# Performance work log

Hardware: AMD Instinct MI355X
Metric: run time of the kernel (lower is better)

## Reference

```python
import jax, jax.numpy as jnp
import numpy as np

B, N, FEAT = 64, 1024, 3
HID, STATE, LAYERS, NTYPES = 64, 32, 2, 10


def setup_inputs() -> dict:
    key = jax.random.key(0)
    ks = jax.random.split(key, 16)
    s = 0.1
    return {
        "task_features": jax.random.normal(ks[0], (B, N, FEAT), jnp.float32),
        "task_types": jax.random.randint(ks[1], (B, N), 0, NTYPES, jnp.int32),
        "prev_state": jnp.zeros((B, STATE), jnp.float32),
        "enc_w1": jax.random.normal(ks[2], (HID, FEAT), jnp.float32) * s,
        "enc_b1": jnp.zeros((HID,), jnp.float32),
        "enc_w2": jax.random.normal(ks[3], (HID, HID), jnp.float32) * s,
        "enc_b2": jnp.zeros((HID,), jnp.float32),
        "contention": jax.random.normal(ks[4], (NTYPES, NTYPES), jnp.float32) * 0.1,
        "gnn_w": jax.random.normal(ks[5], (LAYERS, HID, HID), jnp.float32) * s,
        "gnn_b": jnp.zeros((LAYERS, HID), jnp.float32),
        "gru_w_ih": jax.random.normal(ks[6], (3 * STATE, HID), jnp.float32) * s,
        "gru_w_hh": jax.random.normal(ks[7], (3 * STATE, STATE), jnp.float32) * s,
        "gru_b_ih": jnp.zeros((3 * STATE,), jnp.float32),
        "gru_b_hh": jnp.zeros((3 * STATE,), jnp.float32),
        "head_w1": jax.random.normal(ks[8], (HID, HID + STATE), jnp.float32) * s,
        "head_b1": jnp.zeros((HID,), jnp.float32),
        "head_w2": jax.random.normal(ks[9], (1, HID), jnp.float32) * s,
        "head_b2": jnp.zeros((1,), jnp.float32),
    }


def _forward(task_features, task_types, prev_state, enc_w1, enc_b1, enc_w2, enc_b2,
             contention, gnn_w, gnn_b, gru_w_ih, gru_w_hh, gru_b_ih, gru_b_hh,
             head_w1, head_b1, head_w2, head_b2):
    # task encoder: Linear -> ReLU -> Linear
    emb = jax.nn.relu(task_features @ enc_w1.T + enc_b1) @ enc_w2.T + enc_b2  # (B,N,H)
    # interaction graph: type-pair gather + cosine similarity
    base = contention[task_types[:, :, None], task_types[:, None, :]]  # (B,N,N)
    nrm = emb / jnp.maximum(jnp.linalg.norm(emb, axis=-1, keepdims=True), 1e-12)
    sim = jnp.einsum("bnd,bmd->bnm", nrm, nrm)
    adjacency = jax.nn.sigmoid(base) * sim  # (B,N,N)
    # GNN layers: aggregate + linear + relu
    h = emb
    for l in range(LAYERS):
        agg = jnp.einsum("bnm,bmd->bnd", adjacency, h)
        h = jax.nn.relu((h + agg) @ gnn_w[l].T + gnn_b[l])
    ctx = h.mean(axis=1)  # (B,H)
    # GRUCell (torch semantics)
    gi = ctx @ gru_w_ih.T + gru_b_ih
    gh = prev_state @ gru_w_hh.T + gru_b_hh
    i_r, i_z, i_n = jnp.split(gi, 3, axis=-1)
    h_r, h_z, h_n = jnp.split(gh, 3, axis=-1)
    r = jax.nn.sigmoid(i_r + h_r)
    z = jax.nn.sigmoid(i_z + h_z)
    n = jnp.tanh(i_n + r * h_n)
    new_state = (1.0 - z) * n + z * prev_state  # (B,S)
    # latency head on [h, state]
    st = jnp.broadcast_to(new_state[:, None, :], (h.shape[0], h.shape[1], new_state.shape[-1]))
    combined = jnp.concatenate([h, st], axis=-1)
    lat = jax.nn.relu(combined @ head_w1.T + head_b1) @ head_w2.T + head_b2
    return lat[..., 0], new_state


def reference(task_features, task_types, prev_state, enc_w1, enc_b1, enc_w2, enc_b2,
              contention, gnn_w, gnn_b, gru_w_ih, gru_w_hh, gru_b_ih, gru_b_hh,
              head_w1, head_b1, head_w2, head_b2):
    return _forward(task_features, task_types, prev_state, enc_w1, enc_b1, enc_w2, enc_b2,
                    contention, gnn_w, gnn_b, gru_w_ih, gru_w_hh, gru_b_ih, gru_b_hh,
                    head_w1, head_b1, head_w2, head_b2)
```

## Files before the change

### kernel.cpp

```cpp
#include <hip/hip_runtime.h>
#include <math.h>

#define BB 64
#define NN 1024
#define HID 64
#define STATE 32
#define NTYPES 10

typedef _Float16 f16;
typedef f16 f16x8 __attribute__((ext_vector_type(8)));
typedef f16 f16x4 __attribute__((ext_vector_type(4)));
typedef float f32x4 __attribute__((ext_vector_type(4)));

#define MFMA16(a, b, c) __builtin_amdgcn_mfma_f32_16x16x32_f16(a, b, c, 0, 0, 0)

__device__ __forceinline__ float sigm(float x) { return 1.f / (1.f + expf(-x)); }

__device__ __forceinline__ f16x8 cvt8(float4 a, float4 b) {
    f16x8 r;
    r[0] = (f16)a.x; r[1] = (f16)a.y; r[2] = (f16)a.z; r[3] = (f16)a.w;
    r[4] = (f16)b.x; r[5] = (f16)b.y; r[6] = (f16)b.z; r[7] = (f16)b.w;
    return r;
}
__device__ __forceinline__ unsigned packh2(f16 a, f16 b) {
    union { f16 h[2]; unsigned u; } p;
    p.h[0] = a; p.h[1] = b;
    return p.u;
}

__global__ __launch_bounds__(256) void k_misc(
    const float* __restrict__ w2, const float* __restrict__ gw,
    const float* __restrict__ hw1, f16* __restrict__ out,
    int* __restrict__ cnt, float* __restrict__ ctx)
{
    int p = blockIdx.x * 256 + threadIdx.x;
    if (p < 18432) {
        const float* W; int K, pl;
        if (p < 12288) { int seg = p >> 12; pl = p & 4095; W = (seg == 0) ? w2 : gw + (seg - 1) * 4096; K = 64; }
        else { W = hw1; K = 96; pl = p - 12288; }
        int j = pl & 7, lane = (pl >> 3) & 63, nt = (pl >> 9) & 3, ch = pl >> 11;
        int k = ch * 32 + ((lane >> 4) << 3) + j;
        int o = nt * 16 + (lane & 15);
        out[p] = (f16)W[o * K + k];
        return;
    }
    int q = p - 18432;
    if (q < BB * NTYPES) { cnt[q] = 0; return; }
    q -= BB * NTYPES;
    if (q < BB * HID) ctx[q] = 0.f;
}

__global__ __launch_bounds__(256) void k_encoder(
    const float* __restrict__ feat,
    const float* __restrict__ w1, const float* __restrict__ b1,
    const f16* __restrict__ w2f, const float* __restrict__ b2,
    const int* __restrict__ types, int* __restrict__ idx, int* __restrict__ cnt,
    f16* __restrict__ nrm, float* __restrict__ sclv)
{
    __shared__ f16 w2s[4096];
    __shared__ f16 tmp[4][16 * 72];
    __shared__ float fbuf[4][48];
    int tid = threadIdx.x, wave = tid >> 6, lane = tid & 63;
    int l15 = lane & 15, quad = lane >> 4;
    if (tid < 64) {
        int row = blockIdx.x * 64 + tid;
        int b = row >> 10;
        int t = types[row];
        int pos = atomicAdd(&cnt[b * NTYPES + t], 1);
        idx[(b * NTYPES + t) * NN + pos] = row & (NN - 1);
    }
    { const uint4* s = (const uint4*)w2f; uint4* d = (uint4*)w2s;
      for (int i = tid; i < 512; i += 256) d[i] = s[i]; }
    float w10 = w1[lane * 3], w11 = w1[lane * 3 + 1], w12 = w1[lane * 3 + 2], b1l = b1[lane];
    int tb = blockIdx.x * 64 + wave * 16;
    if (lane < 48) fbuf[wave][lane] = feat[tb * 3 + lane];
    __syncthreads();
    f16* tw = &tmp[wave][0];
#pragma unroll
    for (int r = 0; r < 16; ++r) {
        float x0 = fbuf[wave][r * 3], x1 = fbuf[wave][r * 3 + 1], x2 = fbuf[wave][r * 3 + 2];
        float hv = fmaxf(fmaf(w10, x0, fmaf(w11, x1, fmaf(w12, x2, b1l))), 0.f);
        tw[r * 72 + lane] = (f16)hv;
    }
    __builtin_amdgcn_sched_barrier(0);
    f16x8 a0 = *(const f16x8*)&tw[l15 * 72 + quad * 8];
    f16x8 a1 = *(const f16x8*)&tw[l15 * 72 + 32 + quad * 8];
    const f16x8* bf = (const f16x8*)w2s;
    f32x4 acc[4];
#pragma unroll
    for (int nt = 0; nt < 4; ++nt) {
        f32x4 c = {0.f, 0.f, 0.f, 0.f};
        c = MFMA16(a0, bf[(0 * 4 + nt) * 64 + lane], c);
        c = MFMA16(a1, bf[(1 * 4 + nt) * 64 + lane], c);
        acc[nt] = c;
    }
    float b2c[4];
#pragma unroll
    for (int nt = 0; nt < 4; ++nt) b2c[nt] = b2[nt * 16 + l15];
#pragma unroll
    for (int i = 0; i < 4; ++i) {
        float v[4]; float ss = 0.f;
#pragma unroll
        for (int nt = 0; nt < 4; ++nt) { v[nt] = acc[nt][i] + b2c[nt]; ss = fmaf(v[nt], v[nt], ss); }
        ss += __shfl_xor(ss, 1, 64); ss += __shfl_xor(ss, 2, 64);
        ss += __shfl_xor(ss, 4, 64); ss += __shfl_xor(ss, 8, 64);
        float nm = fmaxf(sqrtf(ss), 1e-12f);
        float rinv = 1.f / nm;
        int grow = tb + quad * 4 + i;
#pragma unroll
        for (int nt = 0; nt < 4; ++nt)
            nrm[(size_t)grow * 64 + nt * 16 + l15] = (f16)(v[nt] * rinv);
        if (l15 == 0) sclv[grow] = nm;
    }
}

#define TSTR 40
__global__ __launch_bounds__(256) void k_buildM(
    const int* __restrict__ idx, const int* __restrict__ cnt,
    const f16* __restrict__ nrm, const f16* __restrict__ h,
    const float* __restrict__ scale, f16* __restrict__ M)
{
    __shared__ f16 nT[64 * TSTR];
    __shared__ f16 hT[64 * TSTR];
    int bj = blockIdx.x;
    int b = bj / NTYPES, j = bj % NTYPES;
    int c = cnt[b * NTYPES + j];
    const int* lst = idx + (size_t)bj * NN;
    int tid = threadIdx.x, wave = tid >> 6, lane = tid & 63;
    int l15 = lane & 15, quad = lane >> 4;
    int r = tid & 15;
    int q4 = tid >> 4;
    const f16* nb = nrm + (size_t)b * NN * 64;
    const f16* hb = h + (size_t)b * NN * 64;
    const float* sb = scale ? scale + (size_t)b * NN : nullptr;
    f32x4 acc[4] = {{0.f,0.f,0.f,0.f},{0.f,0.f,0.f,0.f},{0.f,0.f,0.f,0.f},{0.f,0.f,0.f,0.f}};
    for (int k0 = 0; k0 < c; k0 += 32) {
        __syncthreads();
        int m0i = k0 + 2 * r, m1i = m0i + 1;
        f16x4 a0 = {0,0,0,0}, a1 = {0,0,0,0}, g0 = {0,0,0,0}, g1 = {0,0,0,0};
        if (m0i < c) {
            int m = lst[m0i];
            a0 = *(const f16x4*)&nb[(size_t)m * 64 + 4 * q4];
            if (sb) { f16 sm = (f16)sb[m]; f16x4 sv = {sm, sm, sm, sm}; g0 = a0 * sv; }
            else g0 = *(const f16x4*)&hb[(size_t)m * 64 + 4 * q4];
        }
        if (m1i < c) {
            int m = lst[m1i];
            a1 = *(const f16x4*)&nb[(size_t)m * 64 + 4 * q4];
            if (sb) { f16 sm = (f16)sb[m]; f16x4 sv = {sm, sm, sm, sm}; g1 = a1 * sv; }
            else g1 = *(const f16x4*)&hb[(size_t)m * 64 + 4 * q4];
        }
#pragma unroll
        for (int i = 0; i < 4; ++i) {
            *(unsigned*)&nT[(4 * q4 + i) * TSTR + 2 * r] = packh2(a0[i], a1[i]);
            *(unsigned*)&hT[(4 * q4 + i) * TSTR + 2 * r] = packh2(g0[i], g1[i]);
        }
        __syncthreads();
        f16x8 af = *(const f16x8*)&nT[(wave * 16 + l15) * TSTR + quad * 8];
#pragma unroll
        for (int nt = 0; nt < 4; ++nt) {
            f16x8 bfv = *(const f16x8*)&hT[(nt * 16 + l15) * TSTR + quad * 8];
            acc[nt] = MFMA16(af, bfv, acc[nt]);
        }
    }
    f16* Mo = M + (size_t)bj * 4096;
#pragma unroll
    for (int nt = 0; nt < 4; ++nt)
#pragma unroll
        for (int i = 0; i < 4; ++i)
            Mo[(wave * 16 + quad * 4 + i) * 64 + nt * 16 + l15] = (f16)acc[nt][i];
}

__global__ __launch_bounds__(256) void k_gnn_layer(
    const int* __restrict__ idx, const int* __restrict__ cnt,
    const float* __restrict__ cont, const f16* __restrict__ M,
    const f16* __restrict__ nrm, const f16* __restrict__ h,
    const float* __restrict__ scale,
    const f16* __restrict__ gwf, const float* __restrict__ gb,
    f16* __restrict__ hout, float* __restrict__ ctx)
{
    __shared__ f16 ds_[4096];
    __shared__ f16 gs[4096];
    int bt = blockIdx.x;
    int b = bt / NTYPES, t = bt % NTYPES;
    int c = cnt[bt];
    if (c == 0) return;
    int tid = threadIdx.x, wave = tid >> 6, lane = tid & 63;
    int l15 = lane & 15, quad = lane >> 4;
    { const uint4* s2 = (const uint4*)gwf; uint4* d2 = (uint4*)gs;
      for (int i = tid; i < 512; i += 256) d2[i] = s2[i]; }
    float sg[NTYPES];
#pragma unroll
    for (int j = 0; j < NTYPES; ++j) sg[j] = sigm(cont[t * NTYPES + j]);
    float ca[16];
#pragma unroll
    for (int i = 0; i < 16; ++i) ca[i] = 0.f;
    const f16* Mb = M + (size_t)b * NTYPES * 4096;
#pragma unroll
    for (int j = 0; j < NTYPES; ++j) {
        const f16* Mr = Mb + j * 4096 + (wave * 16 + l15) * 64;
        f16x8 m0 = *(const f16x8*)&Mr[quad * 8];
        f16x8 m1 = *(const f16x8*)&Mr[32 + quad * 8];
        float s = sg[j];
#pragma unroll
        for (int e = 0; e < 8; ++e) {
            ca[e]     = fmaf(s, (float)m0[e], ca[e]);
            ca[8 + e] = fmaf(s, (float)m1[e], ca[8 + e]);
        }
    }
    f16x8 ca0, ca1;
#pragma unroll
    for (int i = 0; i < 8; ++i) { ca0[i] = (f16)ca[i]; ca1[i] = (f16)ca[8 + i]; }
    __syncthreads();
    const f16x8* gbf = (const f16x8*)gs;
#pragma unroll
    for (int nt = 0; nt < 4; ++nt) {
        f32x4 dd = {0.f, 0.f, 0.f, 0.f};
        dd = MFMA16(ca0, gbf[(0 * 4 + nt) * 64 + lane], dd);
        dd = MFMA16(ca1, gbf[(1 * 4 + nt) * 64 + lane], dd);
#pragma unroll
        for (int i = 0; i < 4; ++i) {
            int d = wave * 16 + quad * 4 + i;
            int pos = (((d >> 5) * 4 + nt) * 64 + ((d >> 3) & 3) * 16 + l15) * 8 + (d & 7);
            ds_[pos] = (f16)dd[i];
        }
    }
    __syncthreads();
    float gbl[4];
#pragma unroll
    for (int nt = 0; nt < 4; ++nt) gbl[nt] = gb[nt * 16 + l15];
    const int* lst = idx + (size_t)bt * NN;
    const f16* nb = nrm + (size_t)b * NN * 64;
    const f16* hb = h + (size_t)b * NN * 64;
    const float* sb = scale ? scale + (size_t)b * NN : nullptr;
    f16* hob = hout + (size_t)b * NN * 64;
    const f16x8* dbf = (const f16x8*)ds_;
    float cacc[4] = {0.f, 0.f, 0.f, 0.f};
    for (int g = wave; g * 16 < c; g += 4) {
        int tb = g * 16;
        int rA = tb + l15; if (rA >= c) rA = c - 1;
        int mA = lst[rA];
        const f16* na = nb + (size_t)mA * 64;
        f16x8 a0 = *(const f16x8*)&na[quad * 8];
        f16x8 a1 = *(const f16x8*)&na[32 + quad * 8];
        if (sb) {
            f32x4 acc1[4], acc2[4];
#pragma unroll
            for (int nt = 0; nt < 4; ++nt) {
                f32x4 c1 = {0.f, 0.f, 0.f, 0.f}, c2 = {0.f, 0.f, 0.f, 0.f};
                c1 = MFMA16(a0, dbf[(0 * 4 + nt) * 64 + lane], c1);
                c1 = MFMA16(a1, dbf[(1 * 4 + nt) * 64 + lane], c1);
                c2 = MFMA16(a0, gbf[(0 * 4 + nt) * 64 + lane], c2);
                c2 = MFMA16(a1, gbf[(1 * 4 + nt) * 64 + lane], c2);
                acc1[nt] = c1; acc2[nt] = c2;
            }
#pragma unroll
            for (int i = 0; i < 4; ++i) {
                int rr = tb + quad * 4 + i;
                if (rr < c) {
                    int m = lst[rr];
                    float sm = sb[m];
#pragma unroll
                    for (int nt = 0; nt < 4; ++nt) {
                        float v = fmaxf(fmaf(sm, acc2[nt][i], acc1[nt][i]) + gbl[nt], 0.f);
                        hob[(size_t)m * 64 + nt * 16 + l15] = (f16)v;
                        cacc[nt] += v;
                    }
                }
            }
        } else {
            const f16* ha = hb + (size_t)mA * 64;
            f16x8 h0 = *(const f16x8*)&ha[quad * 8];
            f16x8 h1 = *(const f16x8*)&ha[32 + quad * 8];
            f32x4 acc[4];
#pragma unroll
            for (int nt = 0; nt < 4; ++nt) {
                f32x4 cc = {0.f, 0.f, 0.f, 0.f};
                cc = MFMA16(a0, dbf[(0 * 4 + nt) * 64 + lane], cc);
                cc = MFMA16(a1, dbf[(1 * 4 + nt) * 64 + lane], cc);
                cc = MFMA16(h0, gbf[(0 * 4 + nt) * 64 + lane], cc);
                cc = MFMA16(h1, gbf[(1 * 4 + nt) * 64 + lane], cc);
                acc[nt] = cc;
            }
#pragma unroll
            for (int i = 0; i < 4; ++i) {
                int rr = tb + quad * 4 + i;
                if (rr < c) {
                    int m = lst[rr];
#pragma unroll
                    for (int nt = 0; nt < 4; ++nt) {
                        float v = fmaxf(acc[nt][i] + gbl[nt], 0.f);
                        hob[(size_t)m * 64 + nt * 16 + l15] = (f16)v;
                        cacc[nt] += v;
                    }
                }
            }
        }
    }
    if (ctx) {
#pragma unroll
        for (int nt = 0; nt < 4; ++nt) {
            float sv = cacc[nt];
            sv += __shfl_xor(sv, 16, 64);
            sv += __shfl_xor(sv, 32, 64);
            if (quad == 0) atomicAdd(&ctx[b * HID + nt * 16 + l15], sv);
        }
    }
}

__global__ __launch_bounds__(256) void k_head(
    const f16* __restrict__ h2, const float* __restrict__ ctx_sum,
    const float* __restrict__ prev,
    const float* __restrict__ w_ih, const float* __restrict__ w_hh,
    const float* __restrict__ b_ih, const float* __restrict__ b_hh,
    const f16* __restrict__ hwf, const float* __restrict__ b1,
    const float* __restrict__ w2, const float* __restrict__ b2,
    float* __restrict__ lat, float* __restrict__ state_out)
{
    __shared__ f16 ws_[6144];
    __shared__ __align__(16) float st[STATE];
    __shared__ float cs[HID], ps[STATE], gis[96], ghs[96];
    int tid = threadIdx.x, wave = tid >> 6, lane = tid & 63;
    int l15 = lane & 15, quad = lane >> 4;
    int b = blockIdx.x >> 4;
    { const uint4* s = (const uint4*)hwf; uint4* d = (uint4*)ws_;
      for (int i = tid; i < 768; i += 256) d[i] = s[i]; }
    if (tid < HID) cs[tid] = ctx_sum[b * HID + tid] * (1.f / NN);
    if (tid >= HID && tid < HID + STATE) ps[tid - HID] = prev[b * STATE + tid - HID];
    __syncthreads();
    if (tid < 96) {
        float gi = b_ih[tid];
#pragma unroll 8
        for (int k = 0; k < HID; ++k) gi = fmaf(w_ih[tid * HID + k], cs[k], gi);
        float gh = b_hh[tid];
#pragma unroll
        for (int k = 0; k < STATE; ++k) gh = fmaf(w_hh[tid * STATE + k], ps[k], gh);
        gis[tid] = gi; ghs[tid] = gh;
    }
    __syncthreads();
    if (tid < STATE) {
        float r = sigm(gis[tid] + ghs[tid]);
        float z = sigm(gis[32 + tid] + ghs[32 + tid]);
        float nn = tanhf(gis[64 + tid] + r * ghs[64 + tid]);
        float v = (1.f - z) * nn + z * ps[tid];
        st[tid] = v;
        if ((blockIdx.x & 15) == 0) state_out[b * STATE + tid] = v;
    }
    __syncthreads();
    float b1c[4], w2c[4];
#pragma unroll
    for (int nt = 0; nt < 4; ++nt) { b1c[nt] = b1[nt * 16 + l15]; w2c[nt] = w2[nt * 16 + l15]; }
    float b2v = b2[0];
    int tb = blockIdx.x * 64 + wave * 16;
    int grow = tb + l15;
    const f16* ha = h2 + (size_t)grow * 64;
    f16x8 a0 = *(const f16x8*)&ha[quad * 8];
    f16x8 a1 = *(const f16x8*)&ha[32 + quad * 8];
    const float4* sp = (const float4*)st;
    f16x8 a2 = cvt8(sp[quad * 2], sp[quad * 2 + 1]);
    const f16x8* bf = (const f16x8*)ws_;
    f32x4 acc[4];
#pragma unroll
    for (int nt = 0; nt < 4; ++nt) {
        f32x4 cc = {0.f, 0.f, 0.f, 0.f};
        cc = MFMA16(a0, bf[(0 * 4 + nt) * 64 + lane], cc);
        cc = MFMA16(a1, bf[(1 * 4 + nt) * 64 + lane], cc);
        cc = MFMA16(a2, bf[(2 * 4 + nt) * 64 + lane], cc);
        acc[nt] = cc;
    }
#pragma unroll
    for (int i = 0; i < 4; ++i) {
        float s = 0.f;
#pragma unroll
        for (int nt = 0; nt < 4; ++nt) s = fmaf(fmaxf(acc[nt][i] + b1c[nt], 0.f), w2c[nt], s);
        s += __shfl_xor(s, 1, 64); s += __shfl_xor(s, 2, 64);
        s += __shfl_xor(s, 4, 64); s += __shfl_xor(s, 8, 64);
        if (l15 == 0) lat[tb + quad * 4 + i] = s + b2v;
    }
}

extern "C" void kernel_launch(void* const* d_in, const int* in_sizes, int n_in,
                              void* d_out, int out_size, void* d_ws, size_t ws_size,
                              hipStream_t stream) {
    const float* feat   = (const float*)d_in[0];
    const int*   types  = (const int*)d_in[1];
    const float* prev   = (const float*)d_in[2];
    const float* enc_w1 = (const float*)d_in[3];
    const float* enc_b1 = (const float*)d_in[4];
    const float* enc_w2 = (const float*)d_in[5];
    const float* enc_b2 = (const float*)d_in[6];
    const float* cont   = (const float*)d_in[7];
    const float* gnn_w  = (const float*)d_in[8];
    const float* gnn_b  = (const float*)d_in[9];
    const float* w_ih   = (const float*)d_in[10];
    const float* w_hh   = (const float*)d_in[11];
    const float* b_ih   = (const float*)d_in[12];
    const float* b_hh   = (const float*)d_in[13];
    const float* hw1    = (const float*)d_in[14];
    const float* hb1    = (const float*)d_in[15];
    const float* hw2    = (const float*)d_in[16];
    const float* hb2    = (const float*)d_in[17];
    float* out = (float*)d_out;

    float* ws  = (float*)d_ws;
    f16*   nrm = (f16*)ws;
    f16*   h1  = (f16*)(ws + 2097152);
    f16*   h2  = (f16*)(ws + 4194304);
    float* scl = ws + 6291456;
    int*   idx = (int*)(ws + 6356992);
    int*   cnt = idx + BB * NTYPES * NN;
    f16*   M0  = (f16*)(ws + 7012992);
    f16*   M1  = (f16*)(ws + 8323712);
    f16*   wfrag = (f16*)(ws + 9634432);
    float* ctx   = ws + 9643648;
    f16*   w2f  = wfrag;
    f16*   gw0f = wfrag + 4096;
    f16*   gw1f = wfrag + 8192;
    f16*   hwf  = wfrag + 12288;

    k_misc<<<91, 256, 0, stream>>>(enc_w2, gnn_w, hw1, wfrag, cnt, ctx);
    k_encoder<<<BB * NN / 64, 256, 0, stream>>>(feat, enc_w1, enc_b1, w2f, enc_b2,
                                                types, idx, cnt, nrm, scl);
    k_buildM<<<BB * NTYPES, 256, 0, stream>>>(idx, cnt, nrm, nrm, scl, M0);
    k_gnn_layer<<<BB * NTYPES, 256, 0, stream>>>(idx, cnt, cont, M0, nrm, nrm, scl,
                                                 gw0f, gnn_b, h1, nullptr);
    k_buildM<<<BB * NTYPES, 256, 0, stream>>>(idx, cnt, nrm, h1, nullptr, M1);
    k_gnn_layer<<<BB * NTYPES, 256, 0, stream>>>(idx, cnt, cont, M1, nrm, h1, nullptr,
                                                 gw1f, gnn_b + HID, h2, ctx);
    k_head<<<BB * NN / 64, 256, 0, stream>>>(h2, ctx, prev, w_ih, w_hh, b_ih, b_hh,
                                             hwf, hb1, hw2, hb2, out, out + BB * NN);
}
```

Baseline: 183.2 us.

## Fuse head first-layer projection into last GNN layer, split GNN blocks, widen buildM K-tile

The last GNN layer now multiplies its output rows by the head's first 64 weight columns via an extra MFMA pass, staged through a per-wave LDS tile, and stores that projection instead of h2. The head kernel then only adds a per-batch state projection, applies ReLU and takes a dot product, with no MFMA or weight staging. GNN layer launches double the grid, with two blocks per (batch, type) sharing the row groups, and buildM processes 64 neighbours per iteration. The risks are that each doubled block recomputes the type-aggregate setup and that the extra LDS round trip adds latency in the GNN kernel.

```diff
diff --git a/kernel.cpp b/kernel.cpp
--- a/kernel.cpp
+++ b/kernel.cpp
@@ -16,12 +16,6 @@
 
 __device__ __forceinline__ float sigm(float x) { return 1.f / (1.f + expf(-x)); }
 
-__device__ __forceinline__ f16x8 cvt8(float4 a, float4 b) {
-    f16x8 r;
-    r[0] = (f16)a.x; r[1] = (f16)a.y; r[2] = (f16)a.z; r[3] = (f16)a.w;
-    r[4] = (f16)b.x; r[5] = (f16)b.y; r[6] = (f16)b.z; r[7] = (f16)b.w;
-    return r;
-}
 __device__ __forceinline__ unsigned packh2(f16 a, f16 b) {
     union { f16 h[2]; unsigned u; } p;
     p.h[0] = a; p.h[1] = b;
@@ -114,17 +108,17 @@
     }
 }
 
-#define TSTR 40
+#define TSTR2 72
 __global__ __launch_bounds__(256) void k_buildM(
     const int* __restrict__ idx, const int* __restrict__ cnt,
     const f16* __restrict__ nrm, const f16* __restrict__ h,
     const float* __restrict__ scale, f16* __restrict__ M)
 {
-    __shared__ f16 nT[64 * TSTR];
-    __shared__ f16 hT[64 * TSTR];
+    __shared__ f16 nT[64 * TSTR2];
+    __shared__ f16 hT[64 * TSTR2];
     int bj = blockIdx.x;
-    int b = bj / NTYPES, j = bj % NTYPES;
-    int c = cnt[b * NTYPES + j];
+    int b = bj / NTYPES;
+    int c = cnt[bj];
     const int* lst = idx + (size_t)bj * NN;
     int tid = threadIdx.x, wave = tid >> 6, lane = tid & 63;
     int l15 = lane & 15, quad = lane >> 4;
@@ -134,33 +128,37 @@
     const f16* hb = h + (size_t)b * NN * 64;
     const float* sb = scale ? scale + (size_t)b * NN : nullptr;
     f32x4 acc[4] = {{0.f,0.f,0.f,0.f},{0.f,0.f,0.f,0.f},{0.f,0.f,0.f,0.f},{0.f,0.f,0.f,0.f}};
-    for (int k0 = 0; k0 < c; k0 += 32) {
+    for (int k0 = 0; k0 < c; k0 += 64) {
         __syncthreads();
-        int m0i = k0 + 2 * r, m1i = m0i + 1;
-        f16x4 a0 = {0,0,0,0}, a1 = {0,0,0,0}, g0 = {0,0,0,0}, g1 = {0,0,0,0};
-        if (m0i < c) {
-            int m = lst[m0i];
-            a0 = *(const f16x4*)&nb[(size_t)m * 64 + 4 * q4];
-            if (sb) { f16 sm = (f16)sb[m]; f16x4 sv = {sm, sm, sm, sm}; g0 = a0 * sv; }
-            else g0 = *(const f16x4*)&hb[(size_t)m * 64 + 4 * q4];
-        }
-        if (m1i < c) {
-            int m = lst[m1i];
-            a1 = *(const f16x4*)&nb[(size_t)m * 64 + 4 * q4];
-            if (sb) { f16 sm = (f16)sb[m]; f16x4 sv = {sm, sm, sm, sm}; g1 = a1 * sv; }
-            else g1 = *(const f16x4*)&hb[(size_t)m * 64 + 4 * q4];
+        f16x4 a[4], g[4];
+#pragma unroll
+        for (int u = 0; u < 4; ++u) { a[u] = (f16x4){0,0,0,0}; g[u] = (f16x4){0,0,0,0}; }
+#pragma unroll
+        for (int u = 0; u < 4; ++u) {
+            int mi = k0 + 4 * r + u;
+            if (mi < c) {
+                int m = lst[mi];
+                a[u] = *(const f16x4*)&nb[(size_t)m * 64 + 4 * q4];
+                if (sb) { f16 sm = (f16)sb[m]; f16x4 sv = {sm, sm, sm, sm}; g[u] = a[u] * sv; }
+                else g[u] = *(const f16x4*)&hb[(size_t)m * 64 + 4 * q4];
+            }
         }
 #pragma unroll
         for (int i = 0; i < 4; ++i) {
-            *(unsigned*)&nT[(4 * q4 + i) * TSTR + 2 * r] = packh2(a0[i], a1[i]);
-            *(unsigned*)&hT[(4 * q4 + i) * TSTR + 2 * r] = packh2(g0[i], g1[i]);
+            *(unsigned*)&nT[(4 * q4 + i) * TSTR2 + 4 * r]     = packh2(a[0][i], a[1][i]);
+            *(unsigned*)&nT[(4 * q4 + i) * TSTR2 + 4 * r + 2] = packh2(a[2][i], a[3][i]);
+            *(unsigned*)&hT[(4 * q4 + i) * TSTR2 + 4 * r]     = packh2(g[0][i], g[1][i]);
+            *(unsigned*)&hT[(4 * q4 + i) * TSTR2 + 4 * r + 2] = packh2(g[2][i], g[3][i]);
         }
         __syncthreads();
-        f16x8 af = *(const f16x8*)&nT[(wave * 16 + l15) * TSTR + quad * 8];
+        f16x8 af0 = *(const f16x8*)&nT[(wave * 16 + l15) * TSTR2 + quad * 8];
+        f16x8 af1 = *(const f16x8*)&nT[(wave * 16 + l15) * TSTR2 + 32 + quad * 8];
 #pragma unroll
         for (int nt = 0; nt < 4; ++nt) {
-            f16x8 bfv = *(const f16x8*)&hT[(nt * 16 + l15) * TSTR + quad * 8];
-            acc[nt] = MFMA16(af, bfv, acc[nt]);
+            f16x8 bf0 = *(const f16x8*)&hT[(nt * 16 + l15) * TSTR2 + quad * 8];
+            f16x8 bf1 = *(const f16x8*)&hT[(nt * 16 + l15) * TSTR2 + 32 + quad * 8];
+            acc[nt] = MFMA16(af0, bf0, acc[nt]);
+            acc[nt] = MFMA16(af1, bf1, acc[nt]);
         }
     }
     f16* Mo = M + (size_t)bj * 4096;
@@ -177,11 +175,14 @@
     const f16* __restrict__ nrm, const f16* __restrict__ h,
     const float* __restrict__ scale,
     const f16* __restrict__ gwf, const float* __restrict__ gb,
+    const f16* __restrict__ hw1f,
     f16* __restrict__ hout, float* __restrict__ ctx)
 {
     __shared__ f16 ds_[4096];
     __shared__ f16 gs[4096];
-    int bt = blockIdx.x;
+    __shared__ f16 tmp[4][16 * 72];
+    int blk = blockIdx.x;
+    int s = blk & 1, bt = blk >> 1;
     int b = bt / NTYPES, t = bt % NTYPES;
     int c = cnt[bt];
     if (c == 0) return;
@@ -201,11 +202,11 @@
         const f16* Mr = Mb + j * 4096 + (wave * 16 + l15) * 64;
         f16x8 m0 = *(const f16x8*)&Mr[quad * 8];
         f16x8 m1 = *(const f16x8*)&Mr[32 + quad * 8];
-        float s = sg[j];
+        float sv = sg[j];
 #pragma unroll
         for (int e = 0; e < 8; ++e) {
-            ca[e]     = fmaf(s, (float)m0[e], ca[e]);
-            ca[8 + e] = fmaf(s, (float)m1[e], ca[8 + e]);
+            ca[e]     = fmaf(sv, (float)m0[e], ca[e]);
+            ca[8 + e] = fmaf(sv, (float)m1[e], ca[8 + e]);
         }
     }
     f16x8 ca0, ca1;
@@ -235,8 +236,10 @@
     const float* sb = scale ? scale + (size_t)b * NN : nullptr;
     f16* hob = hout + (size_t)b * NN * 64;
     const f16x8* dbf = (const f16x8*)ds_;
+    const f16x8* hwbf = (const f16x8*)hw1f;
+    f16* tw = &tmp[wave][0];
     float cacc[4] = {0.f, 0.f, 0.f, 0.f};
-    for (int g = wave; g * 16 < c; g += 4) {
+    for (int g = (s << 2) | wave; g * 16 < c; g += 8) {
         int tb = g * 16;
         int rA = tb + l15; if (rA >= c) rA = c - 1;
         int mA = lst[rA];
@@ -264,7 +267,6 @@
                     for (int nt = 0; nt < 4; ++nt) {
                         float v = fmaxf(fmaf(sm, acc2[nt][i], acc1[nt][i]) + gbl[nt], 0.f);
                         hob[(size_t)m * 64 + nt * 16 + l15] = (f16)v;
-                        cacc[nt] += v;
                     }
                 }
             }
@@ -282,19 +284,32 @@
                 cc = MFMA16(h1, gbf[(1 * 4 + nt) * 64 + lane], cc);
                 acc[nt] = cc;
             }
+            int mS[4]; bool ok[4];
 #pragma unroll
             for (int i = 0; i < 4; ++i) {
                 int rr = tb + quad * 4 + i;
-                if (rr < c) {
-                    int m = lst[rr];
-#pragma unroll
-                    for (int nt = 0; nt < 4; ++nt) {
-                        float v = fmaxf(acc[nt][i] + gbl[nt], 0.f);
-                        hob[(size_t)m * 64 + nt * 16 + l15] = (f16)v;
-                        cacc[nt] += v;
-                    }
+                ok[i] = rr < c;
+                mS[i] = lst[ok[i] ? rr : c - 1];
+#pragma unroll
+                for (int nt = 0; nt < 4; ++nt) {
+                    float v = fmaxf(acc[nt][i] + gbl[nt], 0.f);
+                    if (ok[i]) cacc[nt] += v;
+                    tw[(quad * 4 + i) * 72 + nt * 16 + l15] = (f16)v;
                 }
             }
+            __builtin_amdgcn_sched_barrier(0);
+            f16x8 t0 = *(const f16x8*)&tw[l15 * 72 + quad * 8];
+            f16x8 t1 = *(const f16x8*)&tw[l15 * 72 + 32 + quad * 8];
+#pragma unroll
+            for (int nt = 0; nt < 4; ++nt) {
+                f32x4 pp = {0.f, 0.f, 0.f, 0.f};
+                pp = MFMA16(t0, hwbf[(0 * 4 + nt) * 64 + lane], pp);
+                pp = MFMA16(t1, hwbf[(1 * 4 + nt) * 64 + lane], pp);
+#pragma unroll
+                for (int i = 0; i < 4; ++i)
+                    if (ok[i]) hob[(size_t)mS[i] * 64 + nt * 16 + l15] = (f16)pp[i];
+            }
+            __builtin_amdgcn_sched_barrier(0);
         }
     }
     if (ctx) {
@@ -309,24 +324,21 @@
 }
 
 __global__ __launch_bounds__(256) void k_head(
-    const f16* __restrict__ h2, const float* __restrict__ ctx_sum,
+    const f16* __restrict__ P, const float* __restrict__ ctx_sum,
     const float* __restrict__ prev,
     const float* __restrict__ w_ih, const float* __restrict__ w_hh,
     const float* __restrict__ b_ih, const float* __restrict__ b_hh,
-    const f16* __restrict__ hwf, const float* __restrict__ b1,
+    const float* __restrict__ hw1, const float* __restrict__ b1,
     const float* __restrict__ w2, const float* __restrict__ b2,
     float* __restrict__ lat, float* __restrict__ state_out)
 {
-    __shared__ f16 ws_[6144];
-    __shared__ __align__(16) float st[STATE];
-    __shared__ float cs[HID], ps[STATE], gis[96], ghs[96];
-    int tid = threadIdx.x, wave = tid >> 6, lane = tid & 63;
-    int l15 = lane & 15, quad = lane >> 4;
+    __shared__ float st[STATE], cs[HID], ps[STATE], gis[96], ghs[96];
+    __shared__ float stp[HID], w2s[HID];
+    int tid = threadIdx.x;
     int b = blockIdx.x >> 4;
-    { const uint4* s = (const uint4*)hwf; uint4* d = (uint4*)ws_;
-      for (int i = tid; i < 768; i += 256) d[i] = s[i]; }
     if (tid < HID) cs[tid] = ctx_sum[b * HID + tid] * (1.f / NN);
     if (tid >= HID && tid < HID + STATE) ps[tid - HID] = prev[b * STATE + tid - HID];
+    if (tid >= 96 && tid < 96 + HID) w2s[tid - 96] = w2[tid - 96];
     __syncthreads();
     if (tid < 96) {
         float gi = b_ih[tid];
@@ -347,36 +359,31 @@
         if ((blockIdx.x & 15) == 0) state_out[b * STATE + tid] = v;
     }
     __syncthreads();
-    float b1c[4], w2c[4];
-#pragma unroll
-    for (int nt = 0; nt < 4; ++nt) { b1c[nt] = b1[nt * 16 + l15]; w2c[nt] = w2[nt * 16 + l15]; }
+    if (tid < HID) {
+        float a = b1[tid];
+#pragma unroll
+        for (int k = 0; k < STATE; ++k) a = fmaf(hw1[tid * 96 + 64 + k], st[k], a);
+        stp[tid] = a;
+    }
+    __syncthreads();
+    int wave = tid >> 6, lane = tid & 63;
     float b2v = b2[0];
-    int tb = blockIdx.x * 64 + wave * 16;
-    int grow = tb + l15;
-    const f16* ha = h2 + (size_t)grow * 64;
-    f16x8 a0 = *(const f16x8*)&ha[quad * 8];
-    f16x8 a1 = *(const f16x8*)&ha[32 + quad * 8];
-    const float4* sp = (const float4*)st;
-    f16x8 a2 = cvt8(sp[quad * 2], sp[quad * 2 + 1]);
-    const f16x8* bf = (const f16x8*)ws_;
-    f32x4 acc[4];
-#pragma unroll
-    for (int nt = 0; nt < 4; ++nt) {
-        f32x4 cc = {0.f, 0.f, 0.f, 0.f};
-        cc = MFMA16(a0, bf[(0 * 4 + nt) * 64 + lane], cc);
-        cc = MFMA16(a1, bf[(1 * 4 + nt) * 64 + lane], cc);
-        cc = MFMA16(a2, bf[(2 * 4 + nt) * 64 + lane], cc);
-        acc[nt] = cc;
-    }
-#pragma unroll
-    for (int i = 0; i < 4; ++i) {
-        float s = 0.f;
-#pragma unroll
-        for (int nt = 0; nt < 4; ++nt) s = fmaf(fmaxf(acc[nt][i] + b1c[nt], 0.f), w2c[nt], s);
-        s += __shfl_xor(s, 1, 64); s += __shfl_xor(s, 2, 64);
-        s += __shfl_xor(s, 4, 64); s += __shfl_xor(s, 8, 64);
-        if (l15 == 0) lat[tb + quad * 4 + i] = s + b2v;
-    }
+    int row = blockIdx.x * 64 + wave * 16 + (lane >> 2);
+    int cc = (lane & 3) * 16;
+    const f16* pr = P + (size_t)row * 64 + cc;
+    f16x8 p0 = *(const f16x8*)pr;
+    f16x8 p1 = *(const f16x8*)(pr + 8);
+    float sum = 0.f;
+#pragma unroll
+    for (int e = 0; e < 8; ++e) {
+        float u0 = (float)p0[e] + stp[cc + e];
+        sum = fmaf(fmaxf(u0, 0.f), w2s[cc + e], sum);
+        float u1 = (float)p1[e] + stp[cc + 8 + e];
+        sum = fmaf(fmaxf(u1, 0.f), w2s[cc + 8 + e], sum);
+    }
+    sum += __shfl_xor(sum, 1, 64);
+    sum += __shfl_xor(sum, 2, 64);
+    if ((lane & 3) == 0) lat[row] = sum + b2v;
 }
 
 extern "C" void kernel_launch(void* const* d_in, const int* in_sizes, int n_in,
@@ -405,7 +412,7 @@
     float* ws  = (float*)d_ws;
     f16*   nrm = (f16*)ws;
     f16*   h1  = (f16*)(ws + 2097152);
-    f16*   h2  = (f16*)(ws + 4194304);
+    f16*   P   = (f16*)(ws + 4194304);
     float* scl = ws + 6291456;
     int*   idx = (int*)(ws + 6356992);
     int*   cnt = idx + BB * NTYPES * NN;
@@ -422,11 +429,11 @@
     k_encoder<<<BB * NN / 64, 256, 0, stream>>>(feat, enc_w1, enc_b1, w2f, enc_b2,
                                                 types, idx, cnt, nrm, scl);
     k_buildM<<<BB * NTYPES, 256, 0, stream>>>(idx, cnt, nrm, nrm, scl, M0);
-    k_gnn_layer<<<BB * NTYPES, 256, 0, stream>>>(idx, cnt, cont, M0, nrm, nrm, scl,
-                                                 gw0f, gnn_b, h1, nullptr);
+    k_gnn_layer<<<BB * NTYPES * 2, 256, 0, stream>>>(idx, cnt, cont, M0, nrm, nrm, scl,
+                                                     gw0f, gnn_b, nullptr, h1, nullptr);
     k_buildM<<<BB * NTYPES, 256, 0, stream>>>(idx, cnt, nrm, h1, nullptr, M1);
-    k_gnn_layer<<<BB * NTYPES, 256, 0, stream>>>(idx, cnt, cont, M1, nrm, h1, nullptr,
-                                                 gw1f, gnn_b + HID, h2, ctx);
-    k_head<<<BB * NN / 64, 256, 0, stream>>>(h2, ctx, prev, w_ih, w_hh, b_ih, b_hh,
-                                             hwf, hb1, hw2, hb2, out, out + BB * NN);
-}
+    k_gnn_layer<<<BB * NTYPES * 2, 256, 0, stream>>>(idx, cnt, cont, M1, nrm, h1, nullptr,
+                                                     gw1f, gnn_b + HID, hwf, P, ctx);
+    k_head<<<BB * NN / 64, 256, 0, stream>>>(P, ctx, prev, w_ih, w_hh, b_ih, b_hh,
+                                             hw1, hb1, hw2, hb2, out, out + BB * NN);
+}
```

Result: slower. 191.8 us (+4.6%).

## Double buildM K-step to 64, remap GNN blocks per XCD, drop unused ctx sum

Applied to the files above, without the earlier changes.

k_buildM now gathers 64 neighbor rows per iteration instead of 32. Each thread loads four rows, and each wave issues two MFMAs per output tile, so there are half as many barrier rounds and more loads in flight. The LDS row stride grows from 40 to 72. k_gnn_layer remaps block indices so that blocks of the same batch land on the same XCD, which should improve L2 reuse of that batch's M and h data. The ctx partial sum is removed from the scaled (first-layer) path, where it appears unused; this is correct only if that path never feeds ctx.

```diff
diff --git a/kernel.cpp b/kernel.cpp
--- a/kernel.cpp
+++ b/kernel.cpp
@@ -114,17 +114,17 @@
     }
 }
 
-#define TSTR 40
+#define TSTR2 72
 __global__ __launch_bounds__(256) void k_buildM(
     const int* __restrict__ idx, const int* __restrict__ cnt,
     const f16* __restrict__ nrm, const f16* __restrict__ h,
     const float* __restrict__ scale, f16* __restrict__ M)
 {
-    __shared__ f16 nT[64 * TSTR];
-    __shared__ f16 hT[64 * TSTR];
+    __shared__ f16 nT[64 * TSTR2];
+    __shared__ f16 hT[64 * TSTR2];
     int bj = blockIdx.x;
-    int b = bj / NTYPES, j = bj % NTYPES;
-    int c = cnt[b * NTYPES + j];
+    int b = bj / NTYPES;
+    int c = cnt[bj];
     const int* lst = idx + (size_t)bj * NN;
     int tid = threadIdx.x, wave = tid >> 6, lane = tid & 63;
     int l15 = lane & 15, quad = lane >> 4;
@@ -134,33 +134,37 @@
     const f16* hb = h + (size_t)b * NN * 64;
     const float* sb = scale ? scale + (size_t)b * NN : nullptr;
     f32x4 acc[4] = {{0.f,0.f,0.f,0.f},{0.f,0.f,0.f,0.f},{0.f,0.f,0.f,0.f},{0.f,0.f,0.f,0.f}};
-    for (int k0 = 0; k0 < c; k0 += 32) {
+    for (int k0 = 0; k0 < c; k0 += 64) {
         __syncthreads();
-        int m0i = k0 + 2 * r, m1i = m0i + 1;
-        f16x4 a0 = {0,0,0,0}, a1 = {0,0,0,0}, g0 = {0,0,0,0}, g1 = {0,0,0,0};
-        if (m0i < c) {
-            int m = lst[m0i];
-            a0 = *(const f16x4*)&nb[(size_t)m * 64 + 4 * q4];
-            if (sb) { f16 sm = (f16)sb[m]; f16x4 sv = {sm, sm, sm, sm}; g0 = a0 * sv; }
-            else g0 = *(const f16x4*)&hb[(size_t)m * 64 + 4 * q4];
-        }
-        if (m1i < c) {
-            int m = lst[m1i];
-            a1 = *(const f16x4*)&nb[(size_t)m * 64 + 4 * q4];
-            if (sb) { f16 sm = (f16)sb[m]; f16x4 sv = {sm, sm, sm, sm}; g1 = a1 * sv; }
-            else g1 = *(const f16x4*)&hb[(size_t)m * 64 + 4 * q4];
+        f16x4 a[4], g[4];
+#pragma unroll
+        for (int u = 0; u < 4; ++u) { a[u] = (f16x4){0,0,0,0}; g[u] = (f16x4){0,0,0,0}; }
+#pragma unroll
+        for (int u = 0; u < 4; ++u) {
+            int mi = k0 + 4 * r + u;
+            if (mi < c) {
+                int m = lst[mi];
+                a[u] = *(const f16x4*)&nb[(size_t)m * 64 + 4 * q4];
+                if (sb) { f16 sm = (f16)sb[m]; f16x4 sv = {sm, sm, sm, sm}; g[u] = a[u] * sv; }
+                else g[u] = *(const f16x4*)&hb[(size_t)m * 64 + 4 * q4];
+            }
         }
 #pragma unroll
         for (int i = 0; i < 4; ++i) {
-            *(unsigned*)&nT[(4 * q4 + i) * TSTR + 2 * r] = packh2(a0[i], a1[i]);
-            *(unsigned*)&hT[(4 * q4 + i) * TSTR + 2 * r] = packh2(g0[i], g1[i]);
+            *(unsigned*)&nT[(4 * q4 + i) * TSTR2 + 4 * r]     = packh2(a[0][i], a[1][i]);
+            *(unsigned*)&nT[(4 * q4 + i) * TSTR2 + 4 * r + 2] = packh2(a[2][i], a[3][i]);
+            *(unsigned*)&hT[(4 * q4 + i) * TSTR2 + 4 * r]     = packh2(g[0][i], g[1][i]);
+            *(unsigned*)&hT[(4 * q4 + i) * TSTR2 + 4 * r + 2] = packh2(g[2][i], g[3][i]);
         }
         __syncthreads();
-        f16x8 af = *(const f16x8*)&nT[(wave * 16 + l15) * TSTR + quad * 8];
+        f16x8 af0 = *(const f16x8*)&nT[(wave * 16 + l15) * TSTR2 + quad * 8];
+        f16x8 af1 = *(const f16x8*)&nT[(wave * 16 + l15) * TSTR2 + 32 + quad * 8];
 #pragma unroll
         for (int nt = 0; nt < 4; ++nt) {
-            f16x8 bfv = *(const f16x8*)&hT[(nt * 16 + l15) * TSTR + quad * 8];
-            acc[nt] = MFMA16(af, bfv, acc[nt]);
+            f16x8 bf0 = *(const f16x8*)&hT[(nt * 16 + l15) * TSTR2 + quad * 8];
+            f16x8 bf1 = *(const f16x8*)&hT[(nt * 16 + l15) * TSTR2 + 32 + quad * 8];
+            acc[nt] = MFMA16(af0, bf0, acc[nt]);
+            acc[nt] = MFMA16(af1, bf1, acc[nt]);
         }
     }
     f16* Mo = M + (size_t)bj * 4096;
@@ -181,8 +185,11 @@
 {
     __shared__ f16 ds_[4096];
     __shared__ f16 gs[4096];
-    int bt = blockIdx.x;
-    int b = bt / NTYPES, t = bt % NTYPES;
+    int i0 = blockIdx.x;
+    int xcd = i0 & 7, k = i0 >> 3;
+    int b = xcd + 8 * (k / NTYPES);
+    int t = k % NTYPES;
+    int bt = b * NTYPES + t;
     int c = cnt[bt];
     if (c == 0) return;
     int tid = threadIdx.x, wave = tid >> 6, lane = tid & 63;
@@ -201,11 +208,11 @@
         const f16* Mr = Mb + j * 4096 + (wave * 16 + l15) * 64;
         f16x8 m0 = *(const f16x8*)&Mr[quad * 8];
         f16x8 m1 = *(const f16x8*)&Mr[32 + quad * 8];
-        float s = sg[j];
+        float sv = sg[j];
 #pragma unroll
         for (int e = 0; e < 8; ++e) {
-            ca[e]     = fmaf(s, (float)m0[e], ca[e]);
-            ca[8 + e] = fmaf(s, (float)m1[e], ca[8 + e]);
+            ca[e]     = fmaf(sv, (float)m0[e], ca[e]);
+            ca[8 + e] = fmaf(sv, (float)m1[e], ca[8 + e]);
         }
     }
     f16x8 ca0, ca1;
@@ -264,7 +271,6 @@
                     for (int nt = 0; nt < 4; ++nt) {
                         float v = fmaxf(fmaf(sm, acc2[nt][i], acc1[nt][i]) + gbl[nt], 0.f);
                         hob[(size_t)m * 64 + nt * 16 + l15] = (f16)v;
-                        cacc[nt] += v;
                     }
                 }
             }
```

Result: faster. 177.3 us (median of 2 runs) (-3.2%).
